# Performance work log

Measured on AMD Instinct MI355X. Metric: run time of the kernel, lower is better.

The kernel has to match this reference:

```python
import jax, jax.numpy as jnp
import numpy as np

N_ATOMS = 100000
N_PAIRS = 1600000
F_A = 75    # atom input feats
F_P = 14    # pair input feats
H = 50      # all hidden widths
OUT_A = 50
OUT_P = 50


def _glorot(key, shape):
    fan_in, fan_out = shape
    lim = np.sqrt(6.0 / (fan_in + fan_out)).astype(np.float32)
    return jax.random.uniform(key, shape, jnp.float32, -lim, lim)


def setup_inputs() -> dict:
    key = jax.random.key(0)
    ks = jax.random.split(key, 12)
    atom_features = jax.random.normal(ks[0], (N_ATOMS, F_A), jnp.float32)
    pair_features = jax.random.normal(ks[1], (N_PAIRS, F_P), jnp.float32)
    pair_split = jnp.sort(jax.random.randint(ks[2], (N_PAIRS,), 0, N_ATOMS, jnp.int32))
    atom_to_pair = jax.random.randint(ks[3], (N_PAIRS, 2), 0, N_ATOMS, jnp.int32)
    params = {
        "W_AA": _glorot(ks[4], (F_A, H)), "b_AA": jnp.zeros((H,), jnp.float32),
        "W_PA": _glorot(ks[5], (F_P, H)), "b_PA": jnp.zeros((H,), jnp.float32),
        "W_A": _glorot(ks[6], (2 * H, OUT_A)), "b_A": jnp.zeros((OUT_A,), jnp.float32),
        "W_AP": _glorot(ks[7], (2 * F_A, H)), "b_AP": jnp.zeros((H,), jnp.float32),
        "W_PP": _glorot(ks[8], (F_P, H)), "b_PP": jnp.zeros((H,), jnp.float32),
        "W_P": _glorot(ks[9], (2 * H, OUT_P)), "b_P": jnp.zeros((OUT_P,), jnp.float32),
    }
    return dict(atom_features=atom_features, pair_features=pair_features,
                pair_split=pair_split, atom_to_pair=atom_to_pair, **params)


def reference(atom_features, pair_features, pair_split, atom_to_pair,
              W_AA, b_AA, W_PA, b_PA, W_A, b_A,
              W_AP, b_AP, W_PP, b_PP, W_P, b_P):
    act = jax.nn.relu
    # atom -> atom
    AA = act(atom_features @ W_AA + b_AA)                      # [N_atoms, H]
    # pair -> atom (dense then segment-sum over pairs of each atom)
    PA = act(pair_features @ W_PA + b_PA)                      # [N_pairs, H]
    PA = jax.ops.segment_sum(PA, pair_split, num_segments=atom_features.shape[0])
    A = act(jnp.concatenate([AA, PA], axis=1) @ W_A + b_A)     # [N_atoms, OUT_A]
    # atom pair -> pair (symmetrized gather of endpoint atom feats)
    a_ij = atom_features[atom_to_pair].reshape(-1, 2 * atom_features.shape[1])
    a_ji = atom_features[atom_to_pair[:, ::-1]].reshape(-1, 2 * atom_features.shape[1])
    AP = act(a_ij @ W_AP + b_AP) + act(a_ji @ W_AP + b_AP)     # [N_pairs, H]
    # pair -> pair
    PP = act(pair_features @ W_PP + b_PP)                      # [N_pairs, H]
    P = act(jnp.concatenate([AP, PP], axis=1) @ W_P + b_P)     # [N_pairs, OUT_P]
    return A, P
```

## Files before the change

### kernel.cpp

```cpp
#include <hip/hip_runtime.h>

#define N_ATOMS 100000
#define N_PAIRS 1600000
#define F_A 75
#define F_P 14
#define H 50

#define PROJ_BLOCKS (N_ATOMS / 32)
#define RS_BLOCKS   ((N_PAIRS + 255) / 256)
#define SEG_BLOCKS  (N_ATOMS / 4)
#define PO_BLOCKS   2048
#define AOUT_BLOCKS (N_ATOMS / 32)

typedef float f32x2 __attribute__((ext_vector_type(2)));
typedef float f32x4 __attribute__((ext_vector_type(4)));
typedef short bf16x8 __attribute__((ext_vector_type(8)));

__device__ inline unsigned short f2bf(float f) {
    unsigned u = __float_as_uint(f);
    u += 0x7fffu + ((u >> 16) & 1u);
    return (unsigned short)(u >> 16);
}
__device__ inline float bfu(unsigned u, int hi) {
    return __uint_as_float(hi ? (u & 0xffff0000u) : (u << 16));
}

__global__ __launch_bounds__(256) void k_stageA(
    const float* __restrict__ af, const float* __restrict__ W_AA,
    const float* __restrict__ b_AA, const float* __restrict__ W_AP,
    const float* __restrict__ b_AP, const int* __restrict__ split,
    float* __restrict__ AA, unsigned short* __restrict__ X,
    int* __restrict__ row_start)
{
    const int wave = __builtin_amdgcn_readfirstlane(threadIdx.x >> 6);
    const int lane = threadIdx.x & 63;
    const int h = lane < H ? lane : 0;

    if (blockIdx.x < PROJ_BLOCKS) {
        const int base = blockIdx.x * 32 + wave * 8;
        const float bAA = b_AA[h];
        const float bAP = (lane < H) ? b_AP[lane] : 0.f;

        float aa[8], x1[8], x2[8];
        #pragma unroll
        for (int a = 0; a < 8; ++a) { aa[a] = bAA; x1[a] = 0.f; x2[a] = 0.f; }

        for (int c0 = 0; c0 < 72; c0 += 4) {
            f32x4 fv[8];
            #pragma unroll
            for (int a = 0; a < 8; ++a)
                fv[a] = *(const f32x4*)(af + (size_t)(base + a) * F_A + c0);
            #pragma unroll
            for (int cc = 0; cc < 4; ++cc) {
                int c = c0 + cc;
                float waa = W_AA[c * H + h];
                float w1  = W_AP[c * H + h];
                float w2  = W_AP[(F_A + c) * H + h];
                #pragma unroll
                for (int a = 0; a < 8; ++a) {
                    float f = fv[a][cc];
                    aa[a] = fmaf(f, waa, aa[a]);
                    x1[a] = fmaf(f, w1, x1[a]);
                    x2[a] = fmaf(f, w2, x2[a]);
                }
            }
        }
        #pragma unroll
        for (int c = 72; c < F_A; ++c) {
            float waa = W_AA[c * H + h];
            float w1  = W_AP[c * H + h];
            float w2  = W_AP[(F_A + c) * H + h];
            #pragma unroll
            for (int a = 0; a < 8; ++a) {
                float f = af[(size_t)(base + a) * F_A + c];
                aa[a] = fmaf(f, waa, aa[a]);
                x1[a] = fmaf(f, w1, x1[a]);
                x2[a] = fmaf(f, w2, x2[a]);
            }
        }
        #pragma unroll
        for (int a = 0; a < 8; ++a) {
            int atom = base + a;
            if (lane < H) AA[(size_t)atom * H + lane] = fmaxf(aa[a], 0.f);
            unsigned short v1 = (lane < H) ? f2bf(x1[a] + bAP) : (unsigned short)0;
            unsigned short v2 = (lane < H) ? f2bf(x2[a]) : (unsigned short)0;
            unsigned short* Xrow = X + (size_t)atom * 128;
            Xrow[lane]      = v1;
            Xrow[64 + lane] = v2;
        }
    } else {
        int p = (blockIdx.x - PROJ_BLOCKS) * 256 + threadIdx.x;
        if (p >= N_PAIRS) return;
        int s = split[p];
        int sp = (p == 0) ? -1 : split[p - 1];
        for (int a = sp + 1; a <= s; ++a) row_start[a] = p;
        if (p == N_PAIRS - 1)
            for (int a = s + 1; a <= N_ATOMS; ++a) row_start[a] = N_PAIRS;
    }
}

__global__ __launch_bounds__(256, 5) void k_stageB(
    const float* __restrict__ pf, const int* __restrict__ a2p,
    const unsigned short* __restrict__ X,
    const float* __restrict__ W_PP, const float* __restrict__ b_PP,
    const float* __restrict__ W_P, const float* __restrict__ b_P,
    const int* __restrict__ row_start,
    const float* __restrict__ W_PA, const float* __restrict__ b_PA,
    float* __restrict__ PA, float* __restrict__ outP)
{
    __shared__ __align__(16) char smem[26624];

    const int tid  = threadIdx.x;
    const int wave = __builtin_amdgcn_readfirstlane(tid >> 6);
    const int lane = tid & 63;
    const int h = lane < H ? lane : 0;

    const int idx = blockIdx.x;
    const int q = idx / 13, r = idx % 13;
    const bool is_pair = (r == 0) && (q < PO_BLOCKS);

    if (is_pair) {
        const int pair_blk = q;
        uint4* sWf = (uint4*)smem;
        float (*sWPP)[64] = (float(*)[64])(smem + 16384);
        float* sbPP = (float*)(smem + 16384 + 3584);
        float* sT   = (float*)(smem + 16384 + 3584 + 256);

        #pragma unroll
        for (int rr = 0; rr < 4; ++rr) {
            int e = rr * 256 + tid;
            int fid = e >> 6, lane_e = e & 63;
            int s_ = fid >> 2, n_ = fid & 3;
            int col_e = lane_e & 15, gg = lane_e >> 4;
            int k0 = s_ * 32 + gg * 8;
            int c = n_ * 16 + col_e;
            unsigned w[4];
            #pragma unroll
            for (int hh = 0; hh < 4; ++hh) {
                float vlo = 0.f, vhi = 0.f;
                if (c < H) {
                    int k = k0 + 2 * hh;
                    int r0 = (k < 64) ? (k < H ? k : -1) : ((k - 64) < H ? H + (k - 64) : -1);
                    int k2 = k + 1;
                    int r1 = (k2 < 64) ? (k2 < H ? k2 : -1) : ((k2 - 64) < H ? H + (k2 - 64) : -1);
                    if (r0 >= 0) vlo = W_P[r0 * H + c];
                    if (r1 >= 0) vhi = W_P[r1 * H + c];
                }
                w[hh] = (unsigned)f2bf(vlo) | ((unsigned)f2bf(vhi) << 16);
            }
            sWf[e] = make_uint4(w[0], w[1], w[2], w[3]);
        }
        for (int t = tid; t < F_P * 64; t += 256) {
            int c = t >> 6, o = t & 63;
            sWPP[c][o] = (o < H) ? W_PP[c * H + o] : 0.f;
        }
        if (tid < 64) sbPP[tid] = tid < H ? b_PP[tid] : 0.f;
        __syncthreads();

        const int col = lane & 15;
        const int g = lane >> 4;
        float* const myT = sT + wave * 400;

        float bP[4];
        #pragma unroll
        for (int n = 0; n < 4; ++n) {
            int c = n * 16 + col;
            bP[n] = (c < H) ? b_P[c] : 0.f;
        }

        const int NT = N_PAIRS / 16;
        const int step = PO_BLOCKS * 4;

        int t = pair_blk * 4 + wave;
        int2 ij = ((const int2*)a2p)[t * 16 + col];
        while (t < NT) {
            const int t1 = t + step;
            int2 ij1 = ij;
            if (t1 < NT) ij1 = ((const int2*)a2p)[t1 * 16 + col];

            const int pairbase = t * 16;
            const unsigned short* Xi = X + (size_t)ij.x * 128;
            const unsigned short* Xj = X + (size_t)ij.y * 128;

            uint4 A1[2], B2[2], B1[2], A2[2];
            #pragma unroll
            for (int s = 0; s < 2; ++s) {
                int off = s * 32 + g * 8;
                A1[s] = *(const uint4*)(Xi + off);
                B2[s] = *(const uint4*)(Xj + 64 + off);
                B1[s] = *(const uint4*)(Xj + off);
                A2[s] = *(const uint4*)(Xi + 64 + off);
            }

            float pfr[F_P];
            {
                const f32x2* src = (const f32x2*)(pf + (size_t)(pairbase + col) * F_P);
                #pragma unroll
                for (int c = 0; c < 7; ++c) {
                    f32x2 v = __builtin_nontemporal_load(src + c);
                    pfr[2*c] = v.x; pfr[2*c+1] = v.y;
                }
            }

            f32x4 acc[4];
            #pragma unroll
            for (int n = 0; n < 4; ++n) acc[n] = (f32x4){bP[n], bP[n], bP[n], bP[n]};

            #pragma unroll
            for (int s2 = 0; s2 < 2; ++s2) {
                int ob = s2 * 32 + g * 8;
                float pp[8];
                {
                    const f32x4* bb = (const f32x4*)&sbPP[ob];
                    f32x4 b0 = bb[0], b1 = bb[1];
                    pp[0]=b0.x; pp[1]=b0.y; pp[2]=b0.z; pp[3]=b0.w;
                    pp[4]=b1.x; pp[5]=b1.y; pp[6]=b1.z; pp[7]=b1.w;
                }
                #pragma unroll
                for (int c = 0; c < F_P; ++c) {
                    const f32x4* wr = (const f32x4*)&sWPP[c][ob];
                    f32x4 w0 = wr[0], w1 = wr[1];
                    float pc = pfr[c];
                    pp[0]=fmaf(pc,w0.x,pp[0]); pp[1]=fmaf(pc,w0.y,pp[1]);
                    pp[2]=fmaf(pc,w0.z,pp[2]); pp[3]=fmaf(pc,w0.w,pp[3]);
                    pp[4]=fmaf(pc,w1.x,pp[4]); pp[5]=fmaf(pc,w1.y,pp[5]);
                    pp[6]=fmaf(pc,w1.z,pp[6]); pp[7]=fmaf(pc,w1.w,pp[7]);
                }
                union { unsigned u[4]; bf16x8 v; } ap;
                #pragma unroll
                for (int hh = 0; hh < 4; ++hh) {
                    float lo = fmaxf(pp[2*hh], 0.f), hi2 = fmaxf(pp[2*hh+1], 0.f);
                    ap.u[hh] = (unsigned)f2bf(lo) | ((unsigned)f2bf(hi2) << 16);
                }
                int sg = 2 + s2;
                #pragma unroll
                for (int n = 0; n < 4; ++n) {
                    bf16x8 bfr = ((const bf16x8*)sWf)[(sg * 4 + n) * 64 + lane];
                    acc[n] = __builtin_amdgcn_mfma_f32_16x16x32_bf16(ap.v, bfr, acc[n], 0, 0, 0);
                }
            }

            #pragma unroll
            for (int s = 0; s < 2; ++s) {
                const unsigned* a1 = (const unsigned*)&A1[s];
                const unsigned* b2 = (const unsigned*)&B2[s];
                const unsigned* b1 = (const unsigned*)&B1[s];
                const unsigned* a2 = (const unsigned*)&A2[s];
                union { unsigned u[4]; bf16x8 v; } ap;
                #pragma unroll
                for (int hh = 0; hh < 4; ++hh) {
                    float e1l = bfu(a1[hh],0) + bfu(b2[hh],0);
                    float e2l = bfu(b1[hh],0) + bfu(a2[hh],0);
                    float apl = fmaxf(e1l, 0.f) + fmaxf(e2l, 0.f);
                    float e1h = bfu(a1[hh],1) + bfu(b2[hh],1);
                    float e2h = bfu(b1[hh],1) + bfu(a2[hh],1);
                    float aph = fmaxf(e1h, 0.f) + fmaxf(e2h, 0.f);
                    ap.u[hh] = (unsigned)f2bf(apl) | ((unsigned)f2bf(aph) << 16);
                }
                #pragma unroll
                for (int n = 0; n < 4; ++n) {
                    bf16x8 bfr = ((const bf16x8*)sWf)[(s * 4 + n) * 64 + lane];
                    acc[n] = __builtin_amdgcn_mfma_f32_16x16x32_bf16(ap.v, bfr, acc[n], 0, 0, 0);
                }
            }

            float* dst = outP + (size_t)pairbase * H;
            if (g < 2) {
                #pragma unroll
                for (int n = 0; n < 4; ++n) {
                    int c = n * 16 + col;
                    if (c < H) {
                        #pragma unroll
                        for (int qq = 0; qq < 4; ++qq)
                            myT[(g * 4 + qq) * H + c] = fmaxf(acc[n][qq], 0.f);
                    }
                }
            }
            #pragma unroll
            for (int e = 0; e < 4; ++e) {
                int idx2 = e * 64 + lane;
                if (idx2 < 200) {
                    f32x2 v = *(const f32x2*)&myT[idx2 * 2];
                    __builtin_nontemporal_store(v, (f32x2*)(dst + idx2 * 2));
                }
            }
            if (g >= 2) {
                #pragma unroll
                for (int n = 0; n < 4; ++n) {
                    int c = n * 16 + col;
                    if (c < H) {
                        #pragma unroll
                        for (int qq = 0; qq < 4; ++qq)
                            myT[((g - 2) * 4 + qq) * H + c] = fmaxf(acc[n][qq], 0.f);
                    }
                }
            }
            #pragma unroll
            for (int e = 0; e < 4; ++e) {
                int idx2 = e * 64 + lane;
                if (idx2 < 200) {
                    f32x2 v = *(const f32x2*)&myT[idx2 * 2];
                    __builtin_nontemporal_store(v, (f32x2*)(dst + 400 + idx2 * 2));
                }
            }

            ij = ij1;
            t = t1;
        }
    } else {
        const int pairs_below = min(PO_BLOCKS, q + (r > 0 ? 1 : 0));
        const int seg_id = idx - pairs_below;
        const int atom = seg_id * 4 + wave;

        float w[F_P];
        #pragma unroll
        for (int c = 0; c < F_P; ++c) w[c] = W_PA[c * H + h];
        const float bias = b_PA[h];

        const int start = row_start[atom];
        const int end   = row_start[atom + 1];

        float acc = 0.f;
        int p = start;
        for (; p + 4 <= end; p += 4) {
            f32x2 v[4][7];
            #pragma unroll
            for (int rr = 0; rr < 4; ++rr) {
                const f32x2* src = (const f32x2*)(pf + (size_t)(p + rr) * F_P);
                #pragma unroll
                for (int c = 0; c < 7; ++c) v[rr][c] = __builtin_nontemporal_load(src + c);
            }
            #pragma unroll
            for (int rr = 0; rr < 4; ++rr) {
                float s0 = bias;
                #pragma unroll
                for (int c = 0; c < 7; ++c) {
                    s0 = fmaf(v[rr][c].x, w[2*c], s0);
                    s0 = fmaf(v[rr][c].y, w[2*c+1], s0);
                }
                acc += fmaxf(s0, 0.f);
            }
        }
        for (; p < end; ++p) {
            const f32x2* src = (const f32x2*)(pf + (size_t)p * F_P);
            float s0 = bias;
            #pragma unroll
            for (int c = 0; c < 7; ++c) {
                f32x2 v = __builtin_nontemporal_load(src + c);
                s0 = fmaf(v.x, w[2*c], s0); s0 = fmaf(v.y, w[2*c+1], s0);
            }
            acc += fmaxf(s0, 0.f);
        }
        if (lane < H) PA[(size_t)atom * H + lane] = acc;
    }
}

__global__ __launch_bounds__(256) void k_atom_out(
    const float* __restrict__ AA, const float* __restrict__ PA,
    const float* __restrict__ W_A, const float* __restrict__ b_A,
    float* __restrict__ outA)
{
    __shared__ float sW[2 * H * H];
    __shared__ float sb[H];
    for (int t = threadIdx.x; t < 2 * H * H; t += 256) sW[t] = W_A[t];
    if (threadIdx.x < H) sb[threadIdx.x] = b_A[threadIdx.x];
    __syncthreads();

    const int wave = __builtin_amdgcn_readfirstlane(threadIdx.x >> 6);
    const int lane = threadIdx.x & 63;
    const int h = lane < H ? lane : 0;
    const int base = blockIdx.x * 32 + wave * 8;

    float acc[8];
    #pragma unroll
    for (int a = 0; a < 8; ++a) acc[a] = sb[h];

    for (int k = 0; k < H; ++k) {
        float wA = sW[k * H + h];
        float wP = sW[(H + k) * H + h];
        #pragma unroll
        for (int a = 0; a < 8; ++a) {
            acc[a] = fmaf(AA[(size_t)(base + a) * H + k], wA, acc[a]);
            acc[a] = fmaf(PA[(size_t)(base + a) * H + k], wP, acc[a]);
        }
    }
    #pragma unroll
    for (int a = 0; a < 8; ++a)
        if (lane < H) outA[(size_t)(base + a) * H + lane] = fmaxf(acc[a], 0.f);
}

extern "C" void kernel_launch(void* const* d_in, const int* in_sizes, int n_in,
                              void* d_out, int out_size, void* d_ws, size_t ws_size,
                              hipStream_t stream) {
    const float* af    = (const float*)d_in[0];
    const float* pfeat = (const float*)d_in[1];
    const int*   split = (const int*)d_in[2];
    const int*   a2p   = (const int*)d_in[3];
    const float* W_AA  = (const float*)d_in[4];
    const float* b_AA  = (const float*)d_in[5];
    const float* W_PA  = (const float*)d_in[6];
    const float* b_PA  = (const float*)d_in[7];
    const float* W_A   = (const float*)d_in[8];
    const float* b_A   = (const float*)d_in[9];
    const float* W_AP  = (const float*)d_in[10];
    const float* b_AP  = (const float*)d_in[11];
    const float* W_PP  = (const float*)d_in[12];
    const float* b_PP  = (const float*)d_in[13];
    const float* W_P   = (const float*)d_in[14];
    const float* b_P   = (const float*)d_in[15];

    float* outA = (float*)d_out;
    float* outP = (float*)d_out + (size_t)N_ATOMS * H;

    unsigned short* X  = (unsigned short*)d_ws;
    float* AA          = (float*)(X + (size_t)N_ATOMS * 128);
    float* PA          = AA + (size_t)N_ATOMS * H;
    int*   row_start   = (int*)(PA + (size_t)N_ATOMS * H);

    k_stageA<<<PROJ_BLOCKS + RS_BLOCKS, 256, 0, stream>>>(
        af, W_AA, b_AA, W_AP, b_AP, split, AA, X, row_start);
    k_stageB<<<PO_BLOCKS + SEG_BLOCKS, 256, 0, stream>>>(
        pfeat, a2p, X, W_PP, b_PP, W_P, b_P, row_start, W_PA, b_PA, PA, outP);
    k_atom_out<<<AOUT_BLOCKS, 256, 0, stream>>>(AA, PA, W_A, b_A, outA);
}
```

Baseline: 451.4 us.

## Fuse atom output projection into segment-sum blocks of stage B

```diff
diff --git a/kernel.cpp b/kernel.cpp
--- a/kernel.cpp
+++ b/kernel.cpp
@@ -10,7 +10,6 @@
 #define RS_BLOCKS   ((N_PAIRS + 255) / 256)
 #define SEG_BLOCKS  (N_ATOMS / 4)
 #define PO_BLOCKS   2048
-#define AOUT_BLOCKS (N_ATOMS / 32)
 
 typedef float f32x2 __attribute__((ext_vector_type(2)));
 typedef float f32x4 __attribute__((ext_vector_type(4)));
@@ -106,7 +105,9 @@
     const float* __restrict__ W_P, const float* __restrict__ b_P,
     const int* __restrict__ row_start,
     const float* __restrict__ W_PA, const float* __restrict__ b_PA,
-    float* __restrict__ PA, float* __restrict__ outP)
+    const float* __restrict__ AA, const float* __restrict__ W_A,
+    const float* __restrict__ b_A,
+    float* __restrict__ outA, float* __restrict__ outP)
 {
     __shared__ __align__(16) char smem[26624];
 
@@ -308,6 +309,11 @@
             t = t1;
         }
     } else {
+        float* sWA = (float*)smem;
+        float* pab = (float*)(smem + 20480);
+        for (int t2 = tid; t2 < 2 * H * H; t2 += 256) sWA[t2] = W_A[t2];
+        __syncthreads();
+
         const int pairs_below = min(PO_BLOCKS, q + (r > 0 ? 1 : 0));
         const int seg_id = idx - pairs_below;
         const int atom = seg_id * 4 + wave;
@@ -351,42 +357,18 @@
             }
             acc += fmaxf(s0, 0.f);
         }
-        if (lane < H) PA[(size_t)atom * H + lane] = acc;
+
+        pab[wave * 64 + lane] = (lane < H) ? acc : 0.f;
+
+        float accA = (lane < H) ? b_A[lane] : 0.f;
+        const float* AArow = AA + (size_t)atom * H;
+        for (int k = 0; k < H; ++k) {
+            float aak = AArow[k];
+            accA = fmaf(aak, sWA[k * H + h], accA);
+            accA = fmaf(pab[wave * 64 + k], sWA[(H + k) * H + h], accA);
+        }
+        if (lane < H) outA[(size_t)atom * H + lane] = fmaxf(accA, 0.f);
     }
-}
-
-__global__ __launch_bounds__(256) void k_atom_out(
-    const float* __restrict__ AA, const float* __restrict__ PA,
-    const float* __restrict__ W_A, const float* __restrict__ b_A,
-    float* __restrict__ outA)
-{
-    __shared__ float sW[2 * H * H];
-    __shared__ float sb[H];
-    for (int t = threadIdx.x; t < 2 * H * H; t += 256) sW[t] = W_A[t];
-    if (threadIdx.x < H) sb[threadIdx.x] = b_A[threadIdx.x];
-    __syncthreads();
-
-    const int wave = __builtin_amdgcn_readfirstlane(threadIdx.x >> 6);
-    const int lane = threadIdx.x & 63;
-    const int h = lane < H ? lane : 0;
-    const int base = blockIdx.x * 32 + wave * 8;
-
-    float acc[8];
-    #pragma unroll
-    for (int a = 0; a < 8; ++a) acc[a] = sb[h];
-
-    for (int k = 0; k < H; ++k) {
-        float wA = sW[k * H + h];
-        float wP = sW[(H + k) * H + h];
-        #pragma unroll
-        for (int a = 0; a < 8; ++a) {
-            acc[a] = fmaf(AA[(size_t)(base + a) * H + k], wA, acc[a]);
-            acc[a] = fmaf(PA[(size_t)(base + a) * H + k], wP, acc[a]);
-        }
-    }
-    #pragma unroll
-    for (int a = 0; a < 8; ++a)
-        if (lane < H) outA[(size_t)(base + a) * H + lane] = fmaxf(acc[a], 0.f);
 }
 
 extern "C" void kernel_launch(void* const* d_in, const int* in_sizes, int n_in,
@@ -414,12 +396,11 @@
 
     unsigned short* X  = (unsigned short*)d_ws;
     float* AA          = (float*)(X + (size_t)N_ATOMS * 128);
-    float* PA          = AA + (size_t)N_ATOMS * H;
-    int*   row_start   = (int*)(PA + (size_t)N_ATOMS * H);
+    int*   row_start   = (int*)(AA + (size_t)N_ATOMS * H);
 
     k_stageA<<<PROJ_BLOCKS + RS_BLOCKS, 256, 0, stream>>>(
         af, W_AA, b_AA, W_AP, b_AP, split, AA, X, row_start);
     k_stageB<<<PO_BLOCKS + SEG_BLOCKS, 256, 0, stream>>>(
-        pfeat, a2p, X, W_PP, b_PP, W_P, b_P, row_start, W_PA, b_PA, PA, outP);
-    k_atom_out<<<AOUT_BLOCKS, 256, 0, stream>>>(AA, PA, W_A, b_A, outA);
+        pfeat, a2p, X, W_PP, b_PP, W_P, b_P, row_start, W_PA, b_PA,
+        AA, W_A, b_A, outA, outP);
 }
```

After: 398.6 us, median of 2. 11.7% less time.
